# Kernel tuning notes

Measured on AMD Instinct MI355X. Metric: run time of the kernel, lower is better.

## Reference

```python
import jax, jax.numpy as jnp
import numpy as np

N_DYADIC = 0  # dyadic refinement order 'n' from SigLoss_MMD.__init__


def _sig_gram(X, Y, n):
    """Gram matrix of signature kernels k(x_i, y_j) via the first-order
    finite-difference PDE scheme used by sig_kernels_f/fb_mmd:
        K[i+1,j+1] = K[i+1,j] + K[i,j+1] + K[i,j]*(<dx_i, dy_j> - 1)
    with dyadically refined increments dx = (x_{t+1}-x_t)/2^n repeated 2^n times.
    X: (A, M, D), Y: (B, N, D) -> returns (A, B) = K[:, :, -1, -1].
    The row recurrence is a cumulative sum, so each PDE row is one cumsum
    (fully vectorized over all (A,B) pairs); lax.scan runs over rows.
    """
    f = 2 ** n
    incX = jnp.repeat((X[:, 1:] - X[:, :-1]) / f, f, axis=1)  # (A, MM, D)
    incY = jnp.repeat((Y[:, 1:] - Y[:, :-1]) / f, f, axis=1)  # (B, NN, D)
    Mmat = jnp.einsum('aid,bjd->abij', incX, incY)            # (A, B, MM, NN)
    A, B, MM, NN = Mmat.shape
    ones_col = jnp.ones((A, B, 1), Mmat.dtype)
    row0 = jnp.ones((A, B, NN + 1), Mmat.dtype)               # K[0, :] = 1

    def step(prev_row, Mrow):  # prev_row: (A,B,NN+1), Mrow: (A,B,NN)
        # K[i+1,j+1] - K[i+1,j] = K[i,j+1] + K[i,j]*(M[i,j]-1)  -> cumsum
        inc = prev_row[..., 1:] + prev_row[..., :-1] * (Mrow - 1.0)
        new_row = jnp.concatenate([ones_col, 1.0 + jnp.cumsum(inc, axis=-1)], axis=-1)
        return new_row, None

    last_row, _ = jax.lax.scan(step, row0, jnp.moveaxis(Mmat, 2, 0))
    return last_row[..., -1]  # (A, B)


def setup_inputs() -> dict:
    key = jax.random.key(0)
    kx, ky = jax.random.split(key)
    A, M, D = 64, 128, 128
    SCALE = 0.025  # keeps increment inner products small so the PDE stays bounded
    X = SCALE * jax.random.normal(kx, (A, M, D), dtype=jnp.float32)
    Y = SCALE * jax.random.normal(ky, (A, M, D), dtype=jnp.float32)
    return {"X": X, "Y": Y}


def reference(X, Y):
    K_XX = _sig_gram(X, X, N_DYADIC)
    K_YY = _sig_gram(Y, Y, N_DYADIC)
    K_XY = _sig_gram(X, Y, N_DYADIC)
    mmd_squared = jnp.mean(K_XX) + jnp.mean(K_YY) - 2.0 * jnp.mean(K_XY)
    return mmd_squared
```

## Files before the change

kernel.cpp:

```cpp
#include <hip/hip_runtime.h>
#include <hip/hip_bf16.h>

#define MM 127
#define CHUNK_U16 4096
#define MAT_U16   16384
#define ARR_U16   1048576
#define QS_STRIDE 136
#define QS_DWORDS (64 * QS_STRIDE)

typedef __attribute__((ext_vector_type(8))) short short8;
typedef __attribute__((ext_vector_type(4))) float floatx4;

__device__ __forceinline__ unsigned int pack_bf16_rne(float a, float b) {
  float2 rr; rr.x = a; rr.y = b;
  __hip_bfloat162 hp = __float22bfloat162_rn(rr);
  unsigned int hu; __builtin_memcpy(&hu, &hp, 4);
  return hu;
}

__device__ __forceinline__ float wave_shr1(float x) {
  return __int_as_float(__builtin_amdgcn_update_dpp(
      0, __float_as_int(x), 0x138, 0xf, 0xf, true));
}

__global__ __launch_bounds__(256) void prep_kernel(
    const float* __restrict__ X, const float* __restrict__ Y,
    unsigned short* __restrict__ base, float* __restrict__ acc)
{
  if (blockIdx.x == 0 && threadIdx.x == 0) acc[0] = 0.f;
  const int bid = blockIdx.x;
  const int c = bid & 3;
  const int m = (bid >> 2) & 63;
  const int isY = bid >> 8;
  const float* src = (isY ? Y : X) + m * 128 * 128;
  unsigned short* dst = base + isY * ARR_U16 + m * MAT_U16 + c * CHUNK_U16;

  for (int s = threadIdx.x; s < 512; s += 256) {
    const int r = s >> 2;
    const int g = (s & 3) ^ ((r >> 1) & 3);
    uint4 hv = make_uint4(0, 0, 0, 0);
    if (r < MM) {
      const float* p = src + r * 128 + c * 32 + g * 8;
      float4 u0 = *reinterpret_cast<const float4*>(p);
      float4 u1 = *reinterpret_cast<const float4*>(p + 4);
      float4 v0 = *reinterpret_cast<const float4*>(p + 128);
      float4 v1 = *reinterpret_cast<const float4*>(p + 132);
      hv.x = pack_bf16_rne(v0.x - u0.x, v0.y - u0.y);
      hv.y = pack_bf16_rne(v0.z - u0.z, v0.w - u0.w);
      hv.z = pack_bf16_rne(v1.x - u1.x, v1.y - u1.y);
      hv.w = pack_bf16_rne(v1.z - u1.z, v1.w - u1.w);
    }
    *reinterpret_cast<uint4*>(dst + s * 8) = hv;
  }
}

__global__ __launch_bounds__(256, 4) void sig_pair_kernel(
    const unsigned short* __restrict__ base, float* __restrict__ acc)
{
  __shared__ unsigned int smw[QS_DWORDS];
  unsigned short* const sm = reinterpret_cast<unsigned short*>(smw);
  const int tid = threadIdx.x;
  const int bid = blockIdx.x;

  float w;
  int a, b, srcA, srcB;
  if (bid < 4160) {
    int p = bid;
    srcA = 0;
    if (p >= 2080) { p -= 2080; srcA = 1; }
    srcB = srcA;
    int ia = (int)((sqrtf(8.0f * (float)p + 1.0f) - 1.0f) * 0.5f);
    while ((ia + 1) * (ia + 2) / 2 <= p) ia++;
    while (ia * (ia + 1) / 2 > p) ia--;
    int ib = p - ia * (ia + 1) / 2;
    a = ia; b = ib;
    w = (a == b ? 1.0f : 2.0f) / 4096.0f;
  } else {
    int p = bid - 4160;
    a = p >> 6; b = p & 63;
    srcA = 0; srcB = 1;
    w = -2.0f / 4096.0f;
  }
  const unsigned short* Am = base + srcA * ARR_U16 + a * MAT_U16;
  const unsigned short* Bm = base + srcB * ARR_U16 + b * MAT_U16;

  const int wid = tid >> 6, lane = tid & 63;
  const int row0 = (wid >> 1) * 64, col0 = (wid & 1) * 64;
  const int lrow = lane & 15, quad = lane >> 4;

  {
    uint4 z = make_uint4(0u, 0u, 0u, 0u);
    uint4* smw4 = reinterpret_cast<uint4*>(smw);
    for (int i = tid; i < QS_DWORDS / 4; i += 256) smw4[i] = z;
  }

  floatx4 acc4[4][4];
#pragma unroll
  for (int tr = 0; tr < 4; ++tr)
#pragma unroll
    for (int tc = 0; tc < 4; ++tc) acc4[tr][tc] = (floatx4){0.f, 0.f, 0.f, 0.f};

#pragma unroll 1
  for (int c = 0; c < 4; ++c) {
    const unsigned short* Ac = Am + c * CHUNK_U16;
    const unsigned short* Bc = Bm + c * CHUNK_U16;
    short8 bh[4];
#pragma unroll
    for (int tc = 0; tc < 4; ++tc) {
      int r = col0 + tc * 16 + lrow;
      int off = r * 32 + ((quad ^ ((r >> 1) & 3)) * 8);
      bh[tc] = *reinterpret_cast<const short8*>(&Bc[off]);
    }
#pragma unroll
    for (int tr = 0; tr < 4; ++tr) {
      int r = row0 + tr * 16 + lrow;
      int off = r * 32 + ((quad ^ ((r >> 1) & 3)) * 8);
      short8 ah = *reinterpret_cast<const short8*>(&Ac[off]);
#pragma unroll
      for (int tc = 0; tc < 4; ++tc)
        acc4[tr][tc] = __builtin_amdgcn_mfma_f32_16x16x32_bf16(ah, bh[tc], acc4[tr][tc], 0, 0, 0);
    }
  }
  __syncthreads();

#pragma unroll
  for (int tr = 0; tr < 4; ++tr) {
    const int im0 = row0 + tr * 16 + quad * 4;
#pragma unroll
    for (int tc = 0; tc < 4; ++tc) {
      const int jm = col0 + tc * 16 + lrow;
      if (jm < MM) {
        const int lt = (jm + 1) >> 1;
        const int half = (jm & 1) ? 0 : 1;
        const int phys0 = im0 + jm + 5 - 4 * (lt >> 1) - 4 * (lt & 1);
        unsigned short* p = &sm[(lt * QS_STRIDE + phys0) * 2 + half];
        unsigned int u01 = pack_bf16_rne(acc4[tr][tc][0], acc4[tr][tc][1]);
        unsigned int u23 = pack_bf16_rne(acc4[tr][tc][2], acc4[tr][tc][3]);
        p[0] = (unsigned short)u01;
        p[2] = (unsigned short)(u01 >> 16);
        p[4] = (unsigned short)u23;
        if (im0 + 3 < MM) p[6] = (unsigned short)(u23 >> 16);
      }
    }
  }
  __syncthreads();

  if (wid == ((bid >> 8) & 3)) {
    const int l = lane;
    const int shift = 4 * (l >> 1) + 4 * (l & 1) - 4;
    const unsigned int lbase = l * QS_STRIDE;

    auto loadg = [&](int g) -> uint4 {
      int pb = 4 * g - shift;
      pb = pb < 0 ? 132 : (pb > 128 ? 128 : pb);
      return *reinterpret_cast<const uint4*>(&smw[lbase + pb]);
    };

    float curE = 1.f, curO = 1.f;
    float npE = (l == 0) ? 0.f : 1.f, npO = 1.f;
    uint4 P0 = loadg(0), P1 = loadg(1);

    for (int g = 0; g < 63; ++g) {
      const uint4 cur = P0;
      P0 = P1;
      if (g < 62) P1 = loadg(g + 2);
      unsigned int uu[4] = {cur.x, cur.y, cur.z, cur.w};
#pragma unroll
      for (int e = 0; e < 4; ++e) {
        unsigned int u = uu[e];
        float mE = __uint_as_float(u << 16) - 1.0f;
        float mO = __uint_as_float(u & 0xFFFF0000u) - 1.0f;
        float ncE = wave_shr1(curO);
        float ncO = curE;
        float vE = (curE + npE * mE) + ncE;
        float vO = (curO + npO * mO) + ncO;
        npE = ncE; npO = ncO;
        curE = vE; curO = vO;
      }
    }
    {
      unsigned int uu[2] = {P0.x, P0.y};
#pragma unroll
      for (int e = 0; e < 2; ++e) {
        unsigned int u = uu[e];
        float mE = __uint_as_float(u << 16) - 1.0f;
        float mO = __uint_as_float(u & 0xFFFF0000u) - 1.0f;
        float ncE = wave_shr1(curO);
        float ncO = curE;
        float vE = (curE + npE * mE) + ncE;
        float vO = (curO + npO * mO) + ncO;
        npE = ncE; npO = ncO;
        curE = vE; curO = vO;
      }
    }
    if (l == 63) atomicAdd(acc, w * curO);
  }
}

__global__ void finalize_kernel(const float* __restrict__ acc,
                                unsigned int* __restrict__ out) {
  float v = acc[0];
  __hip_bfloat16 bv = __float2bfloat16(v);
  unsigned short u;
  __builtin_memcpy(&u, &bv, sizeof(u));
  out[0] = ((unsigned int)u << 16) | (unsigned int)u;
}

extern "C" void kernel_launch(void* const* d_in, const int* in_sizes, int n_in,
                              void* d_out, int out_size, void* d_ws, size_t ws_size,
                              hipStream_t stream) {
  const float* X = (const float*)d_in[0];
  const float* Y = (const float*)d_in[1];
  float* acc = (float*)d_ws;
  unsigned short* base = (unsigned short*)((char*)d_ws + 1024);

  prep_kernel<<<512, 256, 0, stream>>>(X, Y, base, acc);
  sig_pair_kernel<<<8256, 256, 0, stream>>>(base, acc);
  finalize_kernel<<<1, 1, 0, stream>>>(acc, (unsigned int*)d_out);
}
```

Measured before the change: 189.4 us.

## Assign one pair per wavefront instead of one pair per block

Each wavefront now computes the full 128x128 Gram tile for its own pair and then runs the PDE sweep itself, so all four waves do recurrence work instead of one wave while three sit idle. Block-level syncs go away, each wave gets a private LDS buffer, and the B fragments are held in registers across the whole tile. In exchange each block uses four times the LDS and many more registers (launch bounds drop to 1 block), which cuts occupancy, and each wave issues four times the MFMA work.

Result: slower. 210.3 us (+11.1%).

```diff
diff --git a/kernel.cpp b/kernel.cpp
--- a/kernel.cpp
+++ b/kernel.cpp
@@ -54,18 +54,18 @@
   }
 }
 
-__global__ __launch_bounds__(256, 4) void sig_pair_kernel(
+__global__ __launch_bounds__(256, 1) void sig_pair_kernel(
     const unsigned short* __restrict__ base, float* __restrict__ acc)
 {
-  __shared__ unsigned int smw[QS_DWORDS];
-  unsigned short* const sm = reinterpret_cast<unsigned short*>(smw);
+  __shared__ unsigned int smw[4 * QS_DWORDS];
   const int tid = threadIdx.x;
-  const int bid = blockIdx.x;
+  const int wid = tid >> 6, lane = tid & 63;
+  const int p0 = blockIdx.x * 4 + wid;
 
   float w;
   int a, b, srcA, srcB;
-  if (bid < 4160) {
-    int p = bid;
+  if (p0 < 4160) {
+    int p = p0;
     srcA = 0;
     if (p >= 2080) { p -= 2080; srcA = 1; }
     srcB = srcA;
@@ -76,7 +76,7 @@
     a = ia; b = ib;
     w = (a == b ? 1.0f : 2.0f) / 4096.0f;
   } else {
-    int p = bid - 4160;
+    int p = p0 - 4160;
     a = p >> 6; b = p & 63;
     srcA = 0; srcB = 1;
     w = -2.0f / 4096.0f;
@@ -84,68 +84,59 @@
   const unsigned short* Am = base + srcA * ARR_U16 + a * MAT_U16;
   const unsigned short* Bm = base + srcB * ARR_U16 + b * MAT_U16;
 
-  const int wid = tid >> 6, lane = tid & 63;
-  const int row0 = (wid >> 1) * 64, col0 = (wid & 1) * 64;
+  unsigned int* const myw = smw + wid * QS_DWORDS;
+  unsigned short* const mys = reinterpret_cast<unsigned short*>(myw);
   const int lrow = lane & 15, quad = lane >> 4;
 
   {
     uint4 z = make_uint4(0u, 0u, 0u, 0u);
-    uint4* smw4 = reinterpret_cast<uint4*>(smw);
-    for (int i = tid; i < QS_DWORDS / 4; i += 256) smw4[i] = z;
-  }
-
-  floatx4 acc4[4][4];
-#pragma unroll
-  for (int tr = 0; tr < 4; ++tr)
-#pragma unroll
-    for (int tc = 0; tc < 4; ++tc) acc4[tr][tc] = (floatx4){0.f, 0.f, 0.f, 0.f};
+    uint4* w4 = reinterpret_cast<uint4*>(myw);
+    for (int i = lane; i < QS_DWORDS / 4; i += 64) w4[i] = z;
+  }
+
+  short8 bh[8][4];
+#pragma unroll
+  for (int tc = 0; tc < 8; ++tc) {
+    const int r = tc * 16 + lrow;
+    const int ro = r * 32 + ((quad ^ ((r >> 1) & 3)) * 8);
+#pragma unroll
+    for (int c = 0; c < 4; ++c)
+      bh[tc][c] = *reinterpret_cast<const short8*>(&Bm[c * CHUNK_U16 + ro]);
+  }
 
 #pragma unroll 1
-  for (int c = 0; c < 4; ++c) {
-    const unsigned short* Ac = Am + c * CHUNK_U16;
-    const unsigned short* Bc = Bm + c * CHUNK_U16;
-    short8 bh[4];
-#pragma unroll
-    for (int tc = 0; tc < 4; ++tc) {
-      int r = col0 + tc * 16 + lrow;
-      int off = r * 32 + ((quad ^ ((r >> 1) & 3)) * 8);
-      bh[tc] = *reinterpret_cast<const short8*>(&Bc[off]);
-    }
-#pragma unroll
-    for (int tr = 0; tr < 4; ++tr) {
-      int r = row0 + tr * 16 + lrow;
-      int off = r * 32 + ((quad ^ ((r >> 1) & 3)) * 8);
-      short8 ah = *reinterpret_cast<const short8*>(&Ac[off]);
-#pragma unroll
-      for (int tc = 0; tc < 4; ++tc)
-        acc4[tr][tc] = __builtin_amdgcn_mfma_f32_16x16x32_bf16(ah, bh[tc], acc4[tr][tc], 0, 0, 0);
-    }
-  }
-  __syncthreads();
-
-#pragma unroll
-  for (int tr = 0; tr < 4; ++tr) {
-    const int im0 = row0 + tr * 16 + quad * 4;
-#pragma unroll
-    for (int tc = 0; tc < 4; ++tc) {
-      const int jm = col0 + tc * 16 + lrow;
+  for (int tr = 0; tr < 8; ++tr) {
+    const int r = tr * 16 + lrow;
+    const int ro = r * 32 + ((quad ^ ((r >> 1) & 3)) * 8);
+    short8 ah[4];
+#pragma unroll
+    for (int c = 0; c < 4; ++c)
+      ah[c] = *reinterpret_cast<const short8*>(&Am[c * CHUNK_U16 + ro]);
+
+    const int im0 = tr * 16 + quad * 4;
+#pragma unroll
+    for (int tc = 0; tc < 8; ++tc) {
+      floatx4 a4 = (floatx4){0.f, 0.f, 0.f, 0.f};
+#pragma unroll
+      for (int c = 0; c < 4; ++c)
+        a4 = __builtin_amdgcn_mfma_f32_16x16x32_bf16(ah[c], bh[tc][c], a4, 0, 0, 0);
+      const int jm = tc * 16 + lrow;
       if (jm < MM) {
         const int lt = (jm + 1) >> 1;
         const int half = (jm & 1) ? 0 : 1;
         const int phys0 = im0 + jm + 5 - 4 * (lt >> 1) - 4 * (lt & 1);
-        unsigned short* p = &sm[(lt * QS_STRIDE + phys0) * 2 + half];
-        unsigned int u01 = pack_bf16_rne(acc4[tr][tc][0], acc4[tr][tc][1]);
-        unsigned int u23 = pack_bf16_rne(acc4[tr][tc][2], acc4[tr][tc][3]);
-        p[0] = (unsigned short)u01;
-        p[2] = (unsigned short)(u01 >> 16);
-        p[4] = (unsigned short)u23;
-        if (im0 + 3 < MM) p[6] = (unsigned short)(u23 >> 16);
+        unsigned short* pp = &mys[(lt * QS_STRIDE + phys0) * 2 + half];
+        unsigned int u01 = pack_bf16_rne(a4[0], a4[1]);
+        unsigned int u23 = pack_bf16_rne(a4[2], a4[3]);
+        pp[0] = (unsigned short)u01;
+        pp[2] = (unsigned short)(u01 >> 16);
+        pp[4] = (unsigned short)u23;
+        if (im0 + 3 < MM) pp[6] = (unsigned short)(u23 >> 16);
       }
     }
   }
-  __syncthreads();
-
-  if (wid == ((bid >> 8) & 3)) {
+
+  {
     const int l = lane;
     const int shift = 4 * (l >> 1) + 4 * (l & 1) - 4;
     const unsigned int lbase = l * QS_STRIDE;
@@ -153,7 +144,7 @@
     auto loadg = [&](int g) -> uint4 {
       int pb = 4 * g - shift;
       pb = pb < 0 ? 132 : (pb > 128 ? 128 : pb);
-      return *reinterpret_cast<const uint4*>(&smw[lbase + pb]);
+      return *reinterpret_cast<const uint4*>(&myw[lbase + pb]);
     };
 
     float curE = 1.f, curO = 1.f;
@@ -215,6 +206,6 @@
   unsigned short* base = (unsigned short*)((char*)d_ws + 1024);
 
   prep_kernel<<<512, 256, 0, stream>>>(X, Y, base, acc);
-  sig_pair_kernel<<<8256, 256, 0, stream>>>(base, acc);
+  sig_pair_kernel<<<2064, 256, 0, stream>>>(base, acc);
   finalize_kernel<<<1, 1, 0, stream>>>(acc, (unsigned int*)d_out);
 }
```
